# Kernel optimization log

Measured on AMD Instinct MI355X. Metric: run time of the kernel, lower is better.

The kernel has to match this reference:

```python
import jax, jax.numpy as jnp
import numpy as np
from jax import lax

D = 48  # cfg.MAX_DISP // 4 with MAX_DISP = 192


def conv2d(x, w, stride=1):
    return lax.conv_general_dilated(x, w, (stride, stride), [(1, 1), (1, 1)],
                                    dimension_numbers=('NCHW', 'OIHW', 'NCHW'))


def conv3d(x, w):
    return lax.conv_general_dilated(x, w, (1, 1, 1), [(1, 1)] * 3,
                                    dimension_numbers=('NCDHW', 'OIDHW', 'NCDHW'))


def bn(x, s, b):
    # eval-mode BatchNorm folded into per-channel scale/bias
    shape = (1, -1) + (1,) * (x.ndim - 2)
    return x * s.reshape(shape) + b.reshape(shape)


def encoder(x, p):
    x = jax.nn.relu(bn(conv2d(x, p['e_w1'], 2), p['e_s1'], p['e_b1']))
    x = jax.nn.relu(bn(conv2d(x, p['e_w2'], 1), p['e_s2'], p['e_b2']))
    x = jax.nn.relu(bn(conv2d(x, p['e_w3'], 2), p['e_s3'], p['e_b3']))
    x = jax.nn.relu(bn(conv2d(x, p['e_w4'], 1), p['e_s4'], p['e_b4']))
    return x  # [B, 32, H/4, W/4]


def build_corr(fl, fr):
    # cost[b, d, h, w] = mean_c fl[b,c,h,w] * fr[b,c,h,w-d], zero where w < d
    B, C, H, W = fl.shape
    padded = jnp.pad(fr, ((0, 0), (0, 0), (0, 0), (D - 1, 0)))  # zero-pad left

    def body(_, d):
        r = lax.dynamic_slice(padded, (0, 0, 0, D - 1 - d), (B, C, H, W))
        return None, jnp.mean(fl * r, axis=1)

    _, cost = lax.scan(body, None, jnp.arange(D))  # [D, B, H, W]
    return jnp.transpose(cost, (1, 0, 2, 3))  # [B, D, H, W]


def forward(img_l, img_r, p):
    H, W = img_l.shape[2], img_l.shape[3]
    fl = encoder(img_l, p)
    fr = encoder(img_r, p)
    cost = build_corr(fl, fr)
    # 3D cost aggregation: treat cost as [B, 1, D, h, w]
    x = cost[:, None]
    x = jax.nn.relu(bn(conv3d(x, p['a_w1']), p['a_s1'], p['a_b1']))
    x = jax.nn.relu(bn(conv3d(x, p['a_w2']), p['a_s2'], p['a_b2']))
    cost = conv3d(x, p['a_w3'])[:, 0]  # [B, D, h, w]
    prob = jax.nn.softmax(-cost, axis=1)
    idx = jnp.arange(D, dtype=cost.dtype).reshape(1, D, 1, 1)
    disp_low = jnp.sum(prob * idx, axis=1, keepdims=True)  # [B, 1, h, w]
    # upsample (bilinear, align_corners=False semantics) and refine
    disp = jax.image.resize(disp_low, (disp_low.shape[0], 1, H, W), method='bilinear') * 4.0
    disp = jax.nn.relu(bn(conv2d(disp, p['r_w1']), p['r_s1'], p['r_b1']))
    disp = jax.nn.relu(conv2d(disp, p['r_w2']))
    return disp, fl


def setup_inputs() -> dict:
    key = jax.random.key(0)
    ks = jax.random.split(key, 32)
    B, H, W = 4, 384, 768

    def n(k, shape, scale=0.1):
        return jax.random.normal(k, shape, jnp.float32) * scale

    inp = {
        'img_l': n(ks[0], (B, 3, H, W), 1.0),
        'img_r': n(ks[1], (B, 3, H, W), 1.0),
        'e_w1': n(ks[2], (16, 3, 3, 3)),
        'e_w2': n(ks[3], (16, 16, 3, 3)),
        'e_w3': n(ks[4], (32, 16, 3, 3)),
        'e_w4': n(ks[5], (32, 32, 3, 3)),
        'e_s1': 1.0 + n(ks[6], (16,)),
        'e_s2': 1.0 + n(ks[7], (16,)),
        'e_s3': 1.0 + n(ks[8], (32,)),
        'e_s4': 1.0 + n(ks[9], (32,)),
        'e_b1': n(ks[10], (16,)),
        'e_b2': n(ks[11], (16,)),
        'e_b3': n(ks[12], (32,)),
        'e_b4': n(ks[13], (32,)),
        'a_w1': n(ks[14], (8, 1, 3, 3, 3)),
        'a_s1': 1.0 + n(ks[15], (8,)),
        'a_b1': n(ks[16], (8,)),
        'a_w2': n(ks[17], (16, 8, 3, 3, 3)),
        'a_s2': 1.0 + n(ks[18], (16,)),
        'a_b2': n(ks[19], (16,)),
        'a_w3': n(ks[20], (1, 16, 3, 3, 3)),
        'r_w1': n(ks[21], (16, 1, 3, 3)),
        'r_s1': 1.0 + n(ks[22], (16,)),
        'r_b1': n(ks[23], (16,)),
        'r_w2': n(ks[24], (1, 16, 3, 3)),
    }
    return inp


def reference(img_l, img_r, e_w1, e_w2, e_w3, e_w4, e_s1, e_s2, e_s3, e_s4,
              e_b1, e_b2, e_b3, e_b4, a_w1, a_s1, a_b1, a_w2, a_s2, a_b2,
              a_w3, r_w1, r_s1, r_b1, r_w2):
    p = dict(e_w1=e_w1, e_w2=e_w2, e_w3=e_w3, e_w4=e_w4,
             e_s1=e_s1, e_s2=e_s2, e_s3=e_s3, e_s4=e_s4,
             e_b1=e_b1, e_b2=e_b2, e_b3=e_b3, e_b4=e_b4,
             a_w1=a_w1, a_s1=a_s1, a_b1=a_b1, a_w2=a_w2, a_s2=a_s2,
             a_b2=a_b2, a_w3=a_w3, r_w1=r_w1, r_s1=r_s1, r_b1=r_b1,
             r_w2=r_w2)
    return forward(img_l, img_r, p)
```

## Files before the change

kernel.cpp:

```cpp
#include <hip/hip_runtime.h>
#include <hip/hip_bf16.h>

typedef __hip_bfloat16 bf16;
typedef __attribute__((ext_vector_type(8))) short short8v;
typedef __attribute__((ext_vector_type(4))) float f32x4;

static inline int cdiv(long long a, int b){ return (int)((a + b - 1) / b); }

__device__ __forceinline__ float uaf(unsigned u){ return __uint_as_float(u); }
__device__ __forceinline__ float ldf(const bf16* p){ return __bfloat162float(*p); }
__device__ __forceinline__ void stf(bf16* p, float v){ *p = __float2bfloat16(v); }

__device__ __forceinline__ void load4v(const float* p, float& a, float& b, float& c, float& d){
    float4 v = *reinterpret_cast<const float4*>(p); a = v.x; b = v.y; c = v.z; d = v.w;
}
__device__ __forceinline__ unsigned short bfbits(float v){
    bf16 h = __float2bfloat16(v); unsigned short s; __builtin_memcpy(&s, &h, 2); return s;
}

__global__ void halo2d_k(bf16* buf, long long bstride, int nsub, long long sstride,
                         int Hp, int Wp, int Cv)
{
    int z = blockIdx.z;
    bf16* b = buf + (long long)(z / nsub) * bstride + (long long)(z % nsub) * sstride;
    uint4 zz = make_uint4(0, 0, 0, 0);
    int rowV = Wp * Cv;
    int totalV = 2 * rowV + (Hp - 2) * 2 * Cv;
    for (int i = blockIdx.x * 256 + threadIdx.x; i < totalV; i += gridDim.x * 256) {
        long long off;
        if (i < rowV) off = i;
        else if (i < 2 * rowV) off = (long long)(Hp - 1) * rowV + (i - rowV);
        else {
            int k = i - 2 * rowV;
            int h = 1 + k / (2 * Cv);
            int r = k % (2 * Cv);
            int wc = (r < Cv) ? 0 : (Wp - 1);
            off = (long long)h * rowV + (long long)wc * Cv + (r < Cv ? r : r - Cv);
        }
        reinterpret_cast<uint4*>(b)[off] = zz;
    }
}

__global__ void zero_planes_k(bf16* buf, long long bstride, long long planeV, int lastPlane)
{
    int b = blockIdx.z, p = blockIdx.y;
    uint4 zz = make_uint4(0, 0, 0, 0);
    bf16* base = buf + (long long)b * bstride;
    long long pl = p ? (long long)lastPlane * planeV : 0;
    for (long long i = blockIdx.x * 256 + threadIdx.x; i < planeV; i += (long long)gridDim.x * 256)
        reinterpret_cast<uint4*>(base)[pl + i] = zz;
}

#define E12_BS 2396288LL
#define E3_BS  1216768LL

__global__ __launch_bounds__(256) void conv_e1(
    const float* __restrict__ in0, const float* __restrict__ in1,
    const float* __restrict__ w, const float* __restrict__ sc, const float* __restrict__ bi,
    bf16* __restrict__ out)
{
    const int H = 384, W = 768, NW = 96;
    int img = blockIdx.z;
    const float* in = (img >= 4) ? in1 + (long long)(img - 4) * 3 * 294912
                                 : in0 + (long long)img * 3 * 294912;

    __shared__ float wl[432];
    __shared__ float sl[16], bl[16];
    for (int j = threadIdx.x; j < 432; j += 256) {
        int k = j / 16, o = j % 16;
        wl[j] = w[o * 27 + k];
    }
    if (threadIdx.x < 16) { sl[threadIdx.x] = sc[threadIdx.x]; bl[threadIdx.x] = bi[threadIdx.x]; }
    __syncthreads();

    int unit = blockIdx.x * 256 + threadIdx.x;
    int h = unit / NW, wseg = unit % NW, w0 = wseg << 2;
    const long long HW = (long long)H * W;

    float acc[16][4];
#pragma unroll
    for (int o = 0; o < 16; ++o){ acc[o][0]=0.f; acc[o][1]=0.f; acc[o][2]=0.f; acc[o][3]=0.f; }

    for (int ic = 0; ic < 3; ++ic) {
        const float* ip = in + (long long)ic * HW;
#pragma unroll
        for (int kh = 0; kh < 3; ++kh) {
            int ih = 2 * h + kh - 1;
            if (ih < 0 || ih >= H) continue;
            const float* row = ip + (long long)ih * W;
            float x0,x1,x2,x3,x4,x5,x6,x7;
            load4v(row + 2 * w0,     x0, x1, x2, x3);
            load4v(row + 2 * w0 + 4, x4, x5, x6, x7);
            float xm = (w0 > 0) ? row[2 * w0 - 1] : 0.f;
            const float* wk = wl + (ic * 9 + kh * 3) * 16;
#pragma unroll
            for (int o = 0; o < 16; ++o) {
                float wa = wk[o], wb = wk[16 + o], wc = wk[32 + o];
                acc[o][0] = fmaf(xm, wa, fmaf(x0, wb, fmaf(x1, wc, acc[o][0])));
                acc[o][1] = fmaf(x1, wa, fmaf(x2, wb, fmaf(x3, wc, acc[o][1])));
                acc[o][2] = fmaf(x3, wa, fmaf(x4, wb, fmaf(x5, wc, acc[o][2])));
                acc[o][3] = fmaf(x5, wa, fmaf(x6, wb, fmaf(x7, wc, acc[o][3])));
            }
        }
    }
    char* ob = (char*)out + (long long)img * E12_BS;
#pragma unroll
    for (int i = 0; i < 4; ++i) {
        float v[16];
#pragma unroll
        for (int o = 0; o < 16; ++o) v[o] = fmaxf(acc[o][i] * sl[o] + bl[o], 0.f);
        uint4 u0, u1;
        u0.x = (unsigned)bfbits(v[0])  | ((unsigned)bfbits(v[1])  << 16);
        u0.y = (unsigned)bfbits(v[2])  | ((unsigned)bfbits(v[3])  << 16);
        u0.z = (unsigned)bfbits(v[4])  | ((unsigned)bfbits(v[5])  << 16);
        u0.w = (unsigned)bfbits(v[6])  | ((unsigned)bfbits(v[7])  << 16);
        u1.x = (unsigned)bfbits(v[8])  | ((unsigned)bfbits(v[9])  << 16);
        u1.y = (unsigned)bfbits(v[10]) | ((unsigned)bfbits(v[11]) << 16);
        u1.z = (unsigned)bfbits(v[12]) | ((unsigned)bfbits(v[13]) << 16);
        u1.w = (unsigned)bfbits(v[14]) | ((unsigned)bfbits(v[15]) << 16);
        char* p = ob + ((long long)(h + 1) * 386 + (w0 + i + 1)) * 32;
        *reinterpret_cast<uint4*>(p)      = u0;
        *reinterpret_cast<uint4*>(p + 16) = u1;
    }
}

__global__ __launch_bounds__(256) void conv_e2_mfma(
    const bf16* __restrict__ in, const float* __restrict__ w,
    const float* __restrict__ sc, const float* __restrict__ bi,
    bf16* __restrict__ out)
{
    __shared__ short alds[16 * 160];
    __shared__ int offl[20];
    int tid = threadIdx.x;
    for (int j = tid; j < 16 * 160; j += 256) {
        int oc = j / 160, kk = j % 160;
        short v = 0;
        if (kk < 144) { int tap = kk / 16, ic = kk % 16; v = (short)bfbits(w[oc * 144 + ic * 9 + tap]); }
        alds[j] = v;
    }
    if (tid < 20) {
        int c = tid / 4, g = tid % 4;
        int tap = 2 * c + (g >> 1); if (tap > 8) tap = 8;
        offl[tid] = ((tap / 3) * 386 + (tap % 3)) * 32 + (g & 1) * 16;
    }
    __syncthreads();

    int wid = tid >> 6, lane = tid & 63;
    int wt = blockIdx.x * 4 + wid;
    int h = wt / 6, w0 = (wt % 6) * 64;
    int img = blockIdx.z;
    int g = lane >> 4, px = lane & 15;

    const char* bp = (const char*)in + (long long)img * E12_BS
                   + ((long long)h * 386 + (w0 + px)) * 32;
    int offr[5];
#pragma unroll
    for (int c = 0; c < 5; ++c) offr[c] = offl[c * 4 + g];
    short8v af[5];
#pragma unroll
    for (int c = 0; c < 5; ++c)
        af[c] = *reinterpret_cast<const short8v*>(&alds[px * 160 + 32 * c + 8 * g]);

    f32x4 acc[4];
#pragma unroll
    for (int pg = 0; pg < 4; ++pg) {
        f32x4 a = {0.f, 0.f, 0.f, 0.f};
        const char* bpp = bp + pg * 512;
#pragma unroll
        for (int c = 0; c < 5; ++c) {
            short8v bf = *reinterpret_cast<const short8v*>(bpp + offr[c]);
            a = __builtin_amdgcn_mfma_f32_16x16x32_bf16(af[c], bf, a, 0, 0, 0);
        }
        acc[pg] = a;
    }
    char* ob = (char*)out + (long long)img * E12_BS;
#pragma unroll
    for (int pg = 0; pg < 4; ++pg) {
        float v[4];
#pragma unroll
        for (int r = 0; r < 4; ++r) {
            int oc = g * 4 + r;
            v[r] = fmaxf(acc[pg][r] * sc[oc] + bi[oc], 0.f);
        }
        uint2 u;
        u.x = (unsigned)bfbits(v[0]) | ((unsigned)bfbits(v[1]) << 16);
        u.y = (unsigned)bfbits(v[2]) | ((unsigned)bfbits(v[3]) << 16);
        *reinterpret_cast<uint2*>(ob + ((long long)(h + 1) * 386 + (w0 + pg * 16 + px + 1)) * 32 + g * 8) = u;
    }
}

__global__ __launch_bounds__(256) void conv_e3_mfma(
    const bf16* __restrict__ in, const float* __restrict__ w,
    const float* __restrict__ sc, const float* __restrict__ bi,
    bf16* __restrict__ out)
{
    __shared__ short alds[16 * 160];
    __shared__ int offl[20];
    int tid = threadIdx.x;
    int och = blockIdx.y;
    for (int j = tid; j < 16 * 160; j += 256) {
        int oc = j / 160, kk = j % 160;
        short v = 0;
        if (kk < 144) { int tap = kk / 16, ic = kk % 16; v = (short)bfbits(w[(och * 16 + oc) * 144 + ic * 9 + tap]); }
        alds[j] = v;
    }
    if (tid < 20) {
        int c = tid / 4, g = tid % 4;
        int tap = 2 * c + (g >> 1); if (tap > 8) tap = 8;
        offl[tid] = ((tap / 3) * 386 + (tap % 3)) * 32 + (g & 1) * 16;
    }
    __syncthreads();

    int wid = tid >> 6, lane = tid & 63;
    int wt = blockIdx.x * 4 + wid;
    int h = wt / 3, w0 = (wt % 3) * 64;
    int img = blockIdx.z;
    int g = lane >> 4, px = lane & 15;

    const char* bp = (const char*)in + (long long)img * E12_BS
                   + ((long long)(2 * h) * 386 + 2 * (w0 + px)) * 32;
    int offr[5];
#pragma unroll
    for (int c = 0; c < 5; ++c) offr[c] = offl[c * 4 + g];
    short8v af[5];
#pragma unroll
    for (int c = 0; c < 5; ++c)
        af[c] = *reinterpret_cast<const short8v*>(&alds[px * 160 + 32 * c + 8 * g]);

    f32x4 acc[4];
#pragma unroll
    for (int pg = 0; pg < 4; ++pg) {
        f32x4 a = {0.f, 0.f, 0.f, 0.f};
        const char* bpp = bp + pg * 1024;
#pragma unroll
        for (int c = 0; c < 5; ++c) {
            short8v bf = *reinterpret_cast<const short8v*>(bpp + offr[c]);
            a = __builtin_amdgcn_mfma_f32_16x16x32_bf16(af[c], bf, a, 0, 0, 0);
        }
        acc[pg] = a;
    }
    char* ob = (char*)out + (long long)img * E3_BS;
#pragma unroll
    for (int pg = 0; pg < 4; ++pg) {
        float v[4];
#pragma unroll
        for (int r = 0; r < 4; ++r) {
            int oc = och * 16 + g * 4 + r;
            v[r] = fmaxf(acc[pg][r] * sc[oc] + bi[oc], 0.f);
        }
        uint2 u;
        u.x = (unsigned)bfbits(v[0]) | ((unsigned)bfbits(v[1]) << 16);
        u.y = (unsigned)bfbits(v[2]) | ((unsigned)bfbits(v[3]) << 16);
        *reinterpret_cast<uint2*>(ob + ((long long)(h + 1) * 194 + (w0 + pg * 16 + px + 1)) * 64
                                  + och * 32 + g * 8) = u;
    }
}

__global__ __launch_bounds__(256) void conv_e4_mfma(
    const bf16* __restrict__ in, const float* __restrict__ w,
    const float* __restrict__ sc, const float* __restrict__ bi,
    float* __restrict__ fl, float* __restrict__ fr)
{
    __shared__ short alds[16 * 288];
    __shared__ int offl[36];
    int tid = threadIdx.x;
    int och = blockIdx.y;
    for (int j = tid; j < 16 * 288; j += 256) {
        int oc = j / 288, kk = j % 288;
        int tap = kk / 32, ic = kk % 32;
        alds[j] = (short)bfbits(w[(och * 16 + oc) * 288 + ic * 9 + tap]);
    }
    if (tid < 36) {
        int c = tid / 4, g = tid % 4;
        offl[tid] = ((c / 3) * 194 + (c % 3)) * 64 + g * 16;
    }
    __syncthreads();

    int wid = tid >> 6, lane = tid & 63;
    int wt = blockIdx.x * 4 + wid;
    int h = wt / 3, w0 = (wt % 3) * 64;
    int img = blockIdx.z;
    int g = lane >> 4, px = lane & 15;

    const char* bp = (const char*)in + (long long)img * E3_BS
                   + ((long long)h * 194 + (w0 + px)) * 64;
    int offr[9];
#pragma unroll
    for (int c = 0; c < 9; ++c) offr[c] = offl[c * 4 + g];
    short8v af[9];
#pragma unroll
    for (int c = 0; c < 9; ++c)
        af[c] = *reinterpret_cast<const short8v*>(&alds[px * 288 + 32 * c + 8 * g]);

    f32x4 acc[4];
#pragma unroll
    for (int pg = 0; pg < 4; ++pg) {
        f32x4 a = {0.f, 0.f, 0.f, 0.f};
        const char* bpp = bp + pg * 1024;
#pragma unroll
        for (int c = 0; c < 9; ++c) {
            short8v bf = *reinterpret_cast<const short8v*>(bpp + offr[c]);
            a = __builtin_amdgcn_mfma_f32_16x16x32_bf16(af[c], bf, a, 0, 0, 0);
        }
        acc[pg] = a;
    }
    float* dst = (img < 4) ? fl + (long long)img * 32 * 18432
                           : fr + (long long)(img - 4) * 32 * 18432;
#pragma unroll
    for (int pg = 0; pg < 4; ++pg) {
#pragma unroll
        for (int r = 0; r < 4; ++r) {
            int oc = och * 16 + g * 4 + r;
            float v = fmaxf(acc[pg][r] * sc[oc] + bi[oc], 0.f);
            dst[(long long)oc * 18432 + (long long)h * 192 + w0 + pg * 16 + px] = v;
        }
    }
}

#define PB1E 7604800LL
#define PB2E 15209600LL

__global__ __launch_bounds__(256) void conv1_nhwc(
    const float* __restrict__ in, const float* __restrict__ w,
    const float* __restrict__ sc, const float* __restrict__ bi,
    bf16* __restrict__ out)
{
    const int H = 96, W = 192, D = 48, NW = 48;
    int zb = blockIdx.z;
    const float* inz = in + (long long)zb * 884736;
    bf16* outz = out + (long long)zb * PB1E;
    int d = blockIdx.y;
    __shared__ float wl[216];
    __shared__ float sl[8], bl[8];
    for (int j = threadIdx.x; j < 216; j += 256) wl[j] = w[j];
    if (threadIdx.x < 8) { sl[threadIdx.x] = sc[threadIdx.x]; bl[threadIdx.x] = bi[threadIdx.x]; }
    __syncthreads();

    int unit = blockIdx.x * 256 + threadIdx.x;
    int h = unit / NW, wseg = unit % NW, w0 = wseg << 2;
    if (h >= H) return;

    float acc[8][4];
#pragma unroll
    for (int o = 0; o < 8; ++o){ acc[o][0]=0.f; acc[o][1]=0.f; acc[o][2]=0.f; acc[o][3]=0.f; }

#pragma unroll
    for (int kd = 0; kd < 3; ++kd) {
        int id = d + kd - 1;
        if (id < 0 || id >= D) continue;
        const float* plane = inz + (long long)id * H * W;
#pragma unroll
        for (int kh = 0; kh < 3; ++kh) {
            int ih = h + kh - 1;
            if (ih < 0 || ih >= H) continue;
            const float* row = plane + (long long)ih * W;
            float x0,x1,x2,x3;
            load4v(row + w0, x0, x1, x2, x3);
            float xl = (wseg > 0)      ? row[w0 - 1] : 0.f;
            float xr = (wseg < NW - 1) ? row[w0 + 4] : 0.f;
            int kb = kd * 9 + kh * 3;
#pragma unroll
            for (int o = 0; o < 8; ++o) {
                float wa = wl[o*27 + kb], wb = wl[o*27 + kb + 1], wc = wl[o*27 + kb + 2];
                acc[o][0] = fmaf(xl, wa, fmaf(x0, wb, fmaf(x1, wc, acc[o][0])));
                acc[o][1] = fmaf(x0, wa, fmaf(x1, wb, fmaf(x2, wc, acc[o][1])));
                acc[o][2] = fmaf(x1, wa, fmaf(x2, wb, fmaf(x3, wc, acc[o][2])));
                acc[o][3] = fmaf(x2, wa, fmaf(x3, wb, fmaf(xr, wc, acc[o][3])));
            }
        }
    }
#pragma unroll
    for (int i = 0; i < 4; ++i) {
        uint4 u;
        float v[8];
#pragma unroll
        for (int o = 0; o < 8; ++o) v[o] = fmaxf(acc[o][i] * sl[o] + bl[o], 0.f);
        u.x = (unsigned)bfbits(v[0]) | ((unsigned)bfbits(v[1]) << 16);
        u.y = (unsigned)bfbits(v[2]) | ((unsigned)bfbits(v[3]) << 16);
        u.z = (unsigned)bfbits(v[4]) | ((unsigned)bfbits(v[5]) << 16);
        u.w = (unsigned)bfbits(v[6]) | ((unsigned)bfbits(v[7]) << 16);
        long long idx = (((long long)(d + 1) * 98 + (h + 1)) * 194 + (w0 + 1 + i)) * 8;
        *reinterpret_cast<uint4*>(&outz[idx]) = u;
    }
}

__global__ __launch_bounds__(256) void conv2_mfma(
    const bf16* __restrict__ in, const float* __restrict__ w,
    const float* __restrict__ sc, const float* __restrict__ bi,
    bf16* __restrict__ out)
{
    __shared__ short alds[16 * 224];
    __shared__ uint4 sB[6 * 3 * 66];
    __shared__ int offl[28];
    int tid = threadIdx.x;
    int zb = blockIdx.z;
    const bf16* inz = in + (long long)zb * PB1E;
    for (int j = tid; j < 16 * 224; j += 256) {
        int oc = j / 224, kk = j % 224;
        short v = 0;
        if (kk < 216) { int t = kk / 8, ic = kk % 8; v = (short)bfbits(w[(oc * 8 + ic) * 27 + t]); }
        alds[j] = v;
    }
    if (tid < 28) {
        int t = (tid < 27) ? tid : 26;
        int kd = t / 9, kh = (t / 3) % 3, kw = t % 3;
        offl[tid] = (kd * 3 + kh) * 66 + kw;
    }

    int hw = blockIdx.x;
    int h = hw / 3, w0 = (hw % 3) * 64;
    int dq = blockIdx.y * 4;
    for (int j = tid; j < 1188; j += 256) {
        int p = j / 198, rem = j % 198;
        int r = rem / 66, c = rem % 66;
        sB[j] = *reinterpret_cast<const uint4*>(
            inz + (((long long)(dq + p) * 98 + (h + r)) * 194 + (w0 + c)) * 8);
    }
    __syncthreads();

    int wid = tid >> 6, lane = tid & 63;
    int g = lane >> 4, px = lane & 15;
    int d = dq + wid;

    const uint4* sBw = sB + wid * 198;
    int offr[7];
#pragma unroll
    for (int c = 0; c < 7; ++c) offr[c] = offl[4 * c + g];
    short8v af[7];
#pragma unroll
    for (int c = 0; c < 7; ++c)
        af[c] = *reinterpret_cast<const short8v*>(&alds[px * 224 + 32 * c + 8 * g]);

    f32x4 acc[4];
#pragma unroll
    for (int pg = 0; pg < 4; ++pg) {
        f32x4 a = {0.f, 0.f, 0.f, 0.f};
        int col = pg * 16 + px;
#pragma unroll
        for (int c = 0; c < 7; ++c) {
            short8v bf = *reinterpret_cast<const short8v*>(&sBw[offr[c] + col]);
            a = __builtin_amdgcn_mfma_f32_16x16x32_bf16(af[c], bf, a, 0, 0, 0);
        }
        acc[pg] = a;
    }

    char* ob = (char*)(out + (long long)zb * PB2E);
#pragma unroll
    for (int pg = 0; pg < 4; ++pg) {
        float v[4];
#pragma unroll
        for (int r = 0; r < 4; ++r) {
            int oc = g * 4 + r;
            v[r] = fmaxf(acc[pg][r] * sc[oc] + bi[oc], 0.f);
        }
        long long pxi = ((long long)(d + 1) * 98 + h + 1) * 194 + (w0 + pg * 16 + px + 1);
        uint2 u;
        u.x = (unsigned)bfbits(v[0]) | ((unsigned)bfbits(v[1]) << 16);
        u.y = (unsigned)bfbits(v[2]) | ((unsigned)bfbits(v[3]) << 16);
        *reinterpret_cast<uint2*>(ob + pxi * 32 + g * 8) = u;
    }
}

__global__ __launch_bounds__(256) void conv3_nhwc(
    const bf16* __restrict__ in, const float* __restrict__ w,
    float* __restrict__ out)
{
    const int H = 96, W = 192, D = 48, NW = 96;
    __shared__ float wl[27][16];
    for (int j = threadIdx.x; j < 432; j += 256) wl[j / 16][j % 16] = w[(j % 16) * 27 + j / 16];
    __syncthreads();

    int zb = blockIdx.z;
    const bf16* inz = in + (long long)zb * PB2E;
    float* outz = out + (long long)zb * 884736;
    int dl0 = blockIdx.y * 4;
    int unit = blockIdx.x * 256 + threadIdx.x;
    int h = unit / NW, wseg = unit % NW, w0 = wseg * 2;

    float acc[4][2];
#pragma unroll
    for (int o = 0; o < 4; ++o){ acc[o][0]=0.f; acc[o][1]=0.f; }

#pragma unroll
    for (int s = 0; s < 6; ++s) {
        int gid = dl0 - 1 + s;
        if (gid < 0 || gid >= D) continue;
        int il = gid + 1;
        const char* plane = (const char*)inz + (long long)il * 98 * 194 * 32;
#pragma unroll
        for (int kh = 0; kh < 3; ++kh) {
            const char* base = plane + ((long long)(h + kh) * 194 + w0) * 32;
#pragma unroll
            for (int hf = 0; hf < 2; ++hf) {
#pragma unroll
                for (int p = 0; p < 4; ++p) {
                    uint4 q = *reinterpret_cast<const uint4*>(base + p * 32 + hf * 16);
                    float x[8];
                    x[0]=uaf(q.x<<16); x[1]=uaf(q.x&0xffff0000u);
                    x[2]=uaf(q.y<<16); x[3]=uaf(q.y&0xffff0000u);
                    x[4]=uaf(q.z<<16); x[5]=uaf(q.z&0xffff0000u);
                    x[6]=uaf(q.w<<16); x[7]=uaf(q.w&0xffff0000u);
#pragma unroll
                    for (int o = 0; o < 4; ++o) {
                        int kd = s - o;
                        if (kd < 0 || kd > 2) continue;
#pragma unroll
                        for (int kw = 0; kw < 3; ++kw) {
                            int i = p - kw;
                            if (i < 0 || i > 1) continue;
                            const int t = kd * 9 + kh * 3 + kw;
                            float sum = 0.f;
#pragma unroll
                            for (int c = 0; c < 8; ++c) sum = fmaf(x[c], wl[t][hf * 8 + c], sum);
                            acc[o][i] += sum;
                        }
                    }
                }
            }
        }
    }
#pragma unroll
    for (int o = 0; o < 4; ++o) {
        float* op = outz + ((long long)(dl0 + o) * H + h) * W + w0;
        *reinterpret_cast<float2*>(op) = make_float2(acc[o][0], acc[o][1]);
    }
}

__global__ __launch_bounds__(256) void corr2_k(
    const float* __restrict__ fl, const float* __restrict__ fr,
    float* __restrict__ cost)
{
    const int C = 32, D = 48, H = 96, W = 192;
    __shared__ float sfl[64 * 33];
    __shared__ float sfr[111 * 33];

    int w0 = blockIdx.x * 64, h = blockIdx.y, b = blockIdx.z;
    int tid = threadIdx.x;

    for (int j = tid; j < 64 * C; j += 256) {
        int w = j % 64, c = j / 64;
        sfl[w * 33 + c] = fl[(((long long)b * C + c) * H + h) * W + w0 + w];
    }
    for (int j = tid; j < 111 * C; j += 256) {
        int wp = j % 111, c = j / 111;
        int gw = w0 - 47 + wp;
        sfr[wp * 33 + c] = (gw >= 0) ? fr[(((long long)b * C + c) * H + h) * W + gw] : 0.f;
    }
    __syncthreads();

    int w = tid & 63, dg = tid >> 6;
    float flr[32];
#pragma unroll
    for (int c = 0; c < 32; ++c) flr[c] = sfl[w * 33 + c];

    for (int dd = 0; dd < 12; ++dd) {
        int d = dg * 12 + dd;
        int wi = w - d + 47;
        float a = 0.f;
#pragma unroll
        for (int c = 0; c < 32; ++c) a = fmaf(flr[c], sfr[wi * 33 + c], a);
        cost[(((long long)b * D + d) * H + h) * W + w0 + w] = a * (1.0f / 32.0f);
    }
}

__global__ void softdisp_k(const float* __restrict__ c3, float* __restrict__ dl,
                           int B, int H, int W)
{
    const int D = 48;
    long long idx = (long long)blockIdx.x * blockDim.x + threadIdx.x;
    long long total = (long long)B * H * W;
    if (idx >= total) return;
    int b = (int)(idx / ((long long)H * W));
    long long rem = idx % ((long long)H * W);
    const float* p = c3 + ((long long)b * D) * H * W + rem;
    long long st = (long long)H * W;

    float v[48];
    float mn = 1e30f;
#pragma unroll
    for (int d = 0; d < D; ++d) { v[d] = p[d * st]; mn = fminf(mn, v[d]); }
    float se = 0.f, sd = 0.f;
#pragma unroll
    for (int d = 0; d < D; ++d) {
        float e = expf(mn - v[d]);
        se += e;
        sd += e * (float)d;
    }
    dl[idx] = sd / se;
}

__global__ __launch_bounds__(256) void refine_fused(
    const float* __restrict__ dlow, const float* __restrict__ w1,
    const float* __restrict__ s1, const float* __restrict__ b1,
    const float* __restrict__ w2, float* __restrict__ out)
{
    const int H = 384, W = 768, Hl = 96, Wl = 192;
    __shared__ float sdu[20][21];
    __shared__ float smid[18][18][20];
    __shared__ float w1l[144], s1l[16], b1l[16], w2l[144];
    int tid = threadIdx.x;
    if (tid < 144) {
        w1l[tid] = w1[tid];
        int ic = tid / 9, tap = tid % 9;
        w2l[tap * 16 + ic] = w2[tid];
    } else if (tid < 160) {
        s1l[tid - 144] = s1[tid - 144]; b1l[tid - 144] = b1[tid - 144];
    }

    int b = blockIdx.z, h0 = blockIdx.y * 16, w0 = blockIdx.x * 16;
    const float* dlb = dlow + (long long)b * Hl * Wl;
    for (int j = tid; j < 400; j += 256) {
        int i = j / 20, k = j % 20;
        int y = h0 - 2 + i, x = w0 - 2 + k;
        float v = 0.f;
        if (y >= 0 && y < H && x >= 0 && x < W) {
            float sy = (y + 0.5f) * 0.25f - 0.5f;
            float sx = (x + 0.5f) * 0.25f - 0.5f;
            sy = fminf(fmaxf(sy, 0.f), (float)(Hl - 1));
            sx = fminf(fmaxf(sx, 0.f), (float)(Wl - 1));
            int y0 = (int)sy, x0 = (int)sx;
            int y1 = min(y0 + 1, Hl - 1), x1 = min(x0 + 1, Wl - 1);
            float fy = sy - y0, fx = sx - x0;
            v = 4.0f * ((1.f - fy) * ((1.f - fx) * dlb[y0 * Wl + x0] + fx * dlb[y0 * Wl + x1])
                      +        fy  * ((1.f - fx) * dlb[y1 * Wl + x0] + fx * dlb[y1 * Wl + x1]));
        }
        sdu[i][k] = v;
    }
    __syncthreads();

    for (int idx = tid; idx < 324; idx += 256) {
        int i = idx / 18, j = idx % 18;
        int gy = h0 - 1 + i, gx = w0 - 1 + j;
        bool inimg = (gy >= 0 && gy < H && gx >= 0 && gx < W);
        float t[9];
#pragma unroll
        for (int kh = 0; kh < 3; ++kh)
#pragma unroll
            for (int kw = 0; kw < 3; ++kw) t[kh * 3 + kw] = sdu[i + kh][j + kw];
        float m[16];
#pragma unroll
        for (int oc = 0; oc < 16; ++oc) {
            float s = 0.f;
#pragma unroll
            for (int k = 0; k < 9; ++k) s = fmaf(t[k], w1l[oc * 9 + k], s);
            m[oc] = inimg ? fmaxf(s * s1l[oc] + b1l[oc], 0.f) : 0.f;
        }
#pragma unroll
        for (int q = 0; q < 4; ++q)
            *reinterpret_cast<float4*>(&smid[i][j][q * 4]) =
                make_float4(m[q*4], m[q*4+1], m[q*4+2], m[q*4+3]);
    }
    __syncthreads();

    int i = tid >> 4, j = tid & 15;
    float s = 0.f;
#pragma unroll
    for (int kh = 0; kh < 3; ++kh)
#pragma unroll
        for (int kw = 0; kw < 3; ++kw) {
            const float* mp = &smid[i + kh][j + kw][0];
            const float* wp = &w2l[(kh * 3 + kw) * 16];
#pragma unroll
            for (int q = 0; q < 4; ++q) {
                float4 x = *reinterpret_cast<const float4*>(mp + q * 4);
                s = fmaf(x.x, wp[q*4+0], s);
                s = fmaf(x.y, wp[q*4+1], s);
                s = fmaf(x.z, wp[q*4+2], s);
                s = fmaf(x.w, wp[q*4+3], s);
            }
        }
    out[(long long)b * H * W + (long long)(h0 + i) * W + w0 + j] = fmaxf(s, 0.f);
}

extern "C" void kernel_launch(void* const* d_in, const int* in_sizes, int n_in,
                              void* d_out, int out_size, void* d_ws, size_t ws_size,
                              hipStream_t stream)
{
    const float* img_l = (const float*)d_in[0];
    const float* img_r = (const float*)d_in[1];
    const float* e_w1 = (const float*)d_in[2];
    const float* e_w2 = (const float*)d_in[3];
    const float* e_w3 = (const float*)d_in[4];
    const float* e_w4 = (const float*)d_in[5];
    const float* e_s1 = (const float*)d_in[6];
    const float* e_s2 = (const float*)d_in[7];
    const float* e_s3 = (const float*)d_in[8];
    const float* e_s4 = (const float*)d_in[9];
    const float* e_b1 = (const float*)d_in[10];
    const float* e_b2 = (const float*)d_in[11];
    const float* e_b3 = (const float*)d_in[12];
    const float* e_b4 = (const float*)d_in[13];
    const float* a_w1 = (const float*)d_in[14];
    const float* a_s1 = (const float*)d_in[15];
    const float* a_b1 = (const float*)d_in[16];
    const float* a_w2 = (const float*)d_in[17];
    const float* a_s2 = (const float*)d_in[18];
    const float* a_b2 = (const float*)d_in[19];
    const float* a_w3 = (const float*)d_in[20];
    const float* r_w1 = (const float*)d_in[21];
    const float* r_s1 = (const float*)d_in[22];
    const float* r_b1 = (const float*)d_in[23];
    const float* r_w2 = (const float*)d_in[24];

    const int B = 4, H = 384, W = 768, H4 = 96, W4 = 192, D = 48;
    const long long HW4 = (long long)H4 * W4;
    const long long DHW = (long long)D * HW4;
    const long long E12E = E12_BS / 2;
    const long long P1E = 98LL * 194 * 8;
    const long long P2E = 98LL * 194 * 16;

    float* out_disp = (float*)d_out;
    float* FL       = out_disp + 1179648;

    char* ws = (char*)d_ws;
    bf16*  E1pad = (bf16*)(ws + 0);
    bf16*  E2pad = (bf16*)(ws + 19170304);
    bf16*  E3pad = (bf16*)(ws + 38340608);
    float* FR    = (float*)(ws + 48074752);
    float* COST  = (float*)(ws + 0);
    bf16*  C1pad = (bf16*) (ws + 14155776);
    bf16*  C2pad = (bf16*) (ws + 44574976);
    float* C3    = COST;
    float* DL    = (float*)(ws + 166251776);

    dim3 blk(256);

    halo2d_k<<<dim3(10, 1, 16), blk, 0, stream>>>(E1pad, E12E, 1, 0, 194, 386, 2);
    halo2d_k<<<dim3(10, 1, 8),  blk, 0, stream>>>(E3pad, E3_BS / 2, 1, 0, 98, 194, 4);

    conv_e1<<<dim3(72, 1, 8), blk, 0, stream>>>(img_l, img_r, e_w1, e_s1, e_b1, E1pad);
    conv_e2_mfma<<<dim3(288, 1, 8), blk, 0, stream>>>(E1pad, e_w2, e_s2, e_b2, E2pad);
    conv_e3_mfma<<<dim3(72, 2, 8), blk, 0, stream>>>(E2pad, e_w3, e_s3, e_b3, E3pad);
    conv_e4_mfma<<<dim3(72, 2, 8), blk, 0, stream>>>(E3pad, e_w4, e_s4, e_b4, FL, FR);

    corr2_k<<<dim3(3, 96, 4), blk, 0, stream>>>(FL, FR, COST);

    zero_planes_k<<<dim3(75, 2, 2), blk, 0, stream>>>(C1pad, PB1E, P1E / 8, 49);
    halo2d_k<<<dim3(3, 1, 96), blk, 0, stream>>>(C1pad + P1E, PB1E, 48, P1E, 98, 194, 1);
    halo2d_k<<<dim3(5, 1, 192), blk, 0, stream>>>(C2pad + P2E, PB2E, 48, P2E, 98, 194, 2);

    for (int sb = 0; sb < 2; ++sb) {
        conv1_nhwc<<<dim3(18, 48, 2), blk, 0, stream>>>(
            COST + sb * 2 * DHW, a_w1, a_s1, a_b1, C1pad);
        conv2_mfma<<<dim3(288, 12, 2), blk, 0, stream>>>(
            C1pad, a_w2, a_s2, a_b2, C2pad + sb * 2 * PB2E);
    }

    conv3_nhwc<<<dim3(36, 12, 4), blk, 0, stream>>>(C2pad, a_w3, C3);

    softdisp_k<<<cdiv(4LL*H4*W4, 256), blk, 0, stream>>>(C3, DL, B, H4, W4);

    refine_fused<<<dim3(48, 24, 4), blk, 0, stream>>>(
        DL, r_w1, r_s1, r_b1, r_w2, out_disp);
}
```

Measured before the change: 403.5 us.

## Rewrite final 3D conv as MFMA kernel with LDS-staged input tile

The final 16-to-1 channel 3D convolution moves from scalar FMA per thread to bf16 MFMA 16x16x32 instructions. The kernel stages a 6x3x66 pixel input tile in shared memory, and only lane row 0 of the A operand carries weights, so most of the MFMA output is wasted. Zero padding planes for C2pad are now written explicitly so the kernel can load depth halos without branching. The change trades more redundant matrix work and an LDS staging pass for less per-thread ALU work and fewer global loads.

```diff
diff --git a/kernel.cpp b/kernel.cpp
--- a/kernel.cpp
+++ b/kernel.cpp
@@ -461,68 +461,72 @@
     }
 }
 
-__global__ __launch_bounds__(256) void conv3_nhwc(
+__global__ __launch_bounds__(256) void conv3_mfma(
     const bf16* __restrict__ in, const float* __restrict__ w,
     float* __restrict__ out)
 {
-    const int H = 96, W = 192, D = 48, NW = 96;
-    __shared__ float wl[27][16];
-    for (int j = threadIdx.x; j < 432; j += 256) wl[j / 16][j % 16] = w[(j % 16) * 27 + j / 16];
-    __syncthreads();
-
+    __shared__ uint4 sB[6 * 3 * 66 * 2];
+    __shared__ short wlds[448] __attribute__((aligned(16)));
+    __shared__ int offl[56];
+    int tid = threadIdx.x;
     int zb = blockIdx.z;
     const bf16* inz = in + (long long)zb * PB2E;
+
+    for (int j = tid; j < 448; j += 256) {
+        int t = j / 16, ic = j % 16;
+        wlds[j] = (t < 27) ? (short)bfbits(w[ic * 27 + t]) : (short)0;
+    }
+    if (tid < 56) {
+        int c = tid / 4, g = tid % 4;
+        int t = 2 * c + (g >> 1); if (t > 26) t = 26;
+        int off = ((t / 9) * 3 + (t / 3) % 3) * 66 + (t % 3);
+        offl[tid] = off * 2 + (g & 1);
+    }
+
+    int hw = blockIdx.x;
+    int h = hw / 3, w0 = (hw % 3) * 64;
+    int dq = blockIdx.y * 4;
+    const uint4* src = reinterpret_cast<const uint4*>(inz);
+    for (int j = tid; j < 2376; j += 256) {
+        int half = j & 1, pxl = j >> 1;
+        int p = pxl / 198, rem = pxl % 198;
+        int r = rem / 66, c = rem % 66;
+        sB[j] = src[(((long long)(dq + p) * 98 + (h + r)) * 194 + (w0 + c)) * 2 + half];
+    }
+    __syncthreads();
+
+    int wid = tid >> 6, lane = tid & 63;
+    int g = lane >> 4, pxi = lane & 15;
+    const uint4* sBw = sB + wid * 396;
+
+    int offr[14];
+#pragma unroll
+    for (int c = 0; c < 14; ++c) offr[c] = offl[c * 4 + g];
+    short8v af[14];
+    short8v zv = {0,0,0,0,0,0,0,0};
+#pragma unroll
+    for (int c = 0; c < 14; ++c)
+        af[c] = (pxi == 0) ? *reinterpret_cast<const short8v*>(&wlds[32 * c + 8 * g]) : zv;
+
+    f32x4 acc[4];
+#pragma unroll
+    for (int pg = 0; pg < 4; ++pg) {
+        f32x4 a = {0.f, 0.f, 0.f, 0.f};
+        int pcol = (pg * 16 + pxi) * 2;
+#pragma unroll
+        for (int c = 0; c < 14; ++c) {
+            short8v bf = *reinterpret_cast<const short8v*>(&sBw[offr[c] + pcol]);
+            a = __builtin_amdgcn_mfma_f32_16x16x32_bf16(af[c], bf, a, 0, 0, 0);
+        }
+        acc[pg] = a;
+    }
+
     float* outz = out + (long long)zb * 884736;
-    int dl0 = blockIdx.y * 4;
-    int unit = blockIdx.x * 256 + threadIdx.x;
-    int h = unit / NW, wseg = unit % NW, w0 = wseg * 2;
-
-    float acc[4][2];
-#pragma unroll
-    for (int o = 0; o < 4; ++o){ acc[o][0]=0.f; acc[o][1]=0.f; }
-
-#pragma unroll
-    for (int s = 0; s < 6; ++s) {
-        int gid = dl0 - 1 + s;
-        if (gid < 0 || gid >= D) continue;
-        int il = gid + 1;
-        const char* plane = (const char*)inz + (long long)il * 98 * 194 * 32;
-#pragma unroll
-        for (int kh = 0; kh < 3; ++kh) {
-            const char* base = plane + ((long long)(h + kh) * 194 + w0) * 32;
-#pragma unroll
-            for (int hf = 0; hf < 2; ++hf) {
-#pragma unroll
-                for (int p = 0; p < 4; ++p) {
-                    uint4 q = *reinterpret_cast<const uint4*>(base + p * 32 + hf * 16);
-                    float x[8];
-                    x[0]=uaf(q.x<<16); x[1]=uaf(q.x&0xffff0000u);
-                    x[2]=uaf(q.y<<16); x[3]=uaf(q.y&0xffff0000u);
-                    x[4]=uaf(q.z<<16); x[5]=uaf(q.z&0xffff0000u);
-                    x[6]=uaf(q.w<<16); x[7]=uaf(q.w&0xffff0000u);
-#pragma unroll
-                    for (int o = 0; o < 4; ++o) {
-                        int kd = s - o;
-                        if (kd < 0 || kd > 2) continue;
-#pragma unroll
-                        for (int kw = 0; kw < 3; ++kw) {
-                            int i = p - kw;
-                            if (i < 0 || i > 1) continue;
-                            const int t = kd * 9 + kh * 3 + kw;
-                            float sum = 0.f;
-#pragma unroll
-                            for (int c = 0; c < 8; ++c) sum = fmaf(x[c], wl[t][hf * 8 + c], sum);
-                            acc[o][i] += sum;
-                        }
-                    }
-                }
-            }
-        }
-    }
-#pragma unroll
-    for (int o = 0; o < 4; ++o) {
-        float* op = outz + ((long long)(dl0 + o) * H + h) * W + w0;
-        *reinterpret_cast<float2*>(op) = make_float2(acc[o][0], acc[o][1]);
+    if (lane < 16) {
+        long long base = ((long long)(dq + wid) * 96 + h) * 192 + w0 + lane;
+#pragma unroll
+        for (int pg = 0; pg < 4; ++pg)
+            outz[base + pg * 16] = acc[pg][0];
     }
 }
 
@@ -737,6 +741,7 @@
 
     zero_planes_k<<<dim3(75, 2, 2), blk, 0, stream>>>(C1pad, PB1E, P1E / 8, 49);
     halo2d_k<<<dim3(3, 1, 96), blk, 0, stream>>>(C1pad + P1E, PB1E, 48, P1E, 98, 194, 1);
+    zero_planes_k<<<dim3(75, 2, 4), blk, 0, stream>>>(C2pad, PB2E, P2E / 8, 49);
     halo2d_k<<<dim3(5, 1, 192), blk, 0, stream>>>(C2pad + P2E, PB2E, 48, P2E, 98, 194, 2);
 
     for (int sb = 0; sb < 2; ++sb) {
@@ -746,7 +751,7 @@
             C1pad, a_w2, a_s2, a_b2, C2pad + sb * 2 * PB2E);
     }
 
-    conv3_nhwc<<<dim3(36, 12, 4), blk, 0, stream>>>(C2pad, a_w3, C3);
+    conv3_mfma<<<dim3(288, 12, 4), blk, 0, stream>>>(C2pad, a_w3, C3);
 
     softdisp_k<<<cdiv(4LL*H4*W4, 256), blk, 0, stream>>>(C3, DL, B, H4, W4);
 
```

Measured after the change: 394.3 us. -2.3%, faster.
